# Optimization experiments

Measured on AMD Instinct MI355X. Metric: run time of the kernel, lower is better.

## Reference

```python
import jax, jax.numpy as jnp
import numpy as np

N = 50000   # nodes
E = 800000  # edges (avg degree 16)
G = 64      # graphs in batch


def setup_inputs() -> dict:
    key = jax.random.key(0)
    ks = jax.random.split(key, 32)
    w = lambda k, shape, s=0.05: (jax.random.normal(k, shape, jnp.float32) * s)
    inp = {}
    inp["x"] = jax.random.normal(ks[0], (N, 3), jnp.float32)
    inp["edge_index"] = jax.random.randint(ks[1], (2, E), 0, N)
    inp["batch"] = jnp.sort(jax.random.randint(ks[2], (N,), 0, G))
    # TransformerConv 1: in=3, heads=2, d=32 -> out 64 (concat)
    inp["Wq1"] = w(ks[3], (3, 64));  inp["bq1"] = w(ks[4], (64,))
    inp["Wk1"] = w(ks[5], (3, 64));  inp["bk1"] = w(ks[6], (64,))
    inp["Wv1"] = w(ks[7], (3, 64));  inp["bv1"] = w(ks[8], (64,))
    inp["Ws1"] = w(ks[9], (3, 64));  inp["bs1"] = w(ks[10], (64,))
    # TransformerConv 2: in=64, heads=2, d=64 -> out 128 (concat)
    inp["Wq2"] = w(ks[11], (64, 128)); inp["bq2"] = w(ks[12], (128,))
    inp["Wk2"] = w(ks[13], (64, 128)); inp["bk2"] = w(ks[14], (128,))
    inp["Wv2"] = w(ks[15], (64, 128)); inp["bv2"] = w(ks[16], (128,))
    inp["Ws2"] = w(ks[17], (64, 128)); inp["bs2"] = w(ks[18], (128,))
    # MLP head
    inp["W1"] = w(ks[19], (128, 32)); inp["b1"] = w(ks[20], (32,))
    inp["W2"] = w(ks[21], (32, 128)); inp["b2"] = w(ks[22], (128,))
    inp["W3"] = w(ks[23], (128, 40)); inp["b3"] = w(ks[24], (40,))
    return inp


def _transformer_conv(x, src, dst, Wq, bq, Wk, bk, Wv, bv, Ws, bs, H, d):
    """PyG TransformerConv (concat=True, root_weight=True, beta=False)."""
    n = x.shape[0]
    q = (x @ Wq + bq).reshape(n, H, d)
    k = (x @ Wk + bk).reshape(n, H, d)
    v = (x @ Wv + bv).reshape(n, H, d)
    # per-edge attention logits: q_i . k_j / sqrt(d), i=dst, j=src  -> [E, H]
    s = (q[dst] * k[src]).sum(-1) / jnp.sqrt(jnp.float32(d))
    # segment softmax over edges grouped by destination node
    m = jax.ops.segment_max(s, dst, num_segments=n)
    m = jnp.where(jnp.isfinite(m), m, 0.0)
    e = jnp.exp(s - m[dst])
    denom = jax.ops.segment_sum(e, dst, num_segments=n)
    alpha = e / jnp.maximum(denom[dst], 1e-16)
    # scatter-add weighted values
    out = jax.ops.segment_sum(alpha[:, :, None] * v[src], dst, num_segments=n)
    return out.reshape(n, H * d) + x @ Ws + bs  # skip connection


def reference(x, edge_index, batch,
              Wq1, bq1, Wk1, bk1, Wv1, bv1, Ws1, bs1,
              Wq2, bq2, Wk2, bk2, Wv2, bv2, Ws2, bs2,
              W1, b1, W2, b2, W3, b3):
    src, dst = edge_index[0], edge_index[1]
    h = jax.nn.relu(_transformer_conv(x, src, dst, Wq1, bq1, Wk1, bk1,
                                      Wv1, bv1, Ws1, bs1, 2, 32))
    h = jax.nn.relu(_transformer_conv(h, src, dst, Wq2, bq2, Wk2, bk2,
                                      Wv2, bv2, Ws2, bs2, 2, 64))
    # global max pool over graphs
    p = jax.ops.segment_max(h, batch, num_segments=G)
    p = jnp.where(jnp.isfinite(p), p, 0.0)
    x_latent = jax.nn.relu(p @ W1 + b1)
    y = jax.nn.relu(x_latent @ W2 + b2)
    return (y @ W3 + b3, x_latent)
```

## Files before the change

### kernel.cpp

```cpp
#include <hip/hip_runtime.h>
#include <hip/hip_bf16.h>

typedef short s16x8 __attribute__((ext_vector_type(8)));
typedef float f32x4 __attribute__((ext_vector_type(4)));

#define LOG2E 1.4426950408889634f

__device__ __forceinline__ float bfl(unsigned w) { return __uint_as_float(w << 16); }
__device__ __forceinline__ float bfh(unsigned w) { return __uint_as_float(w & 0xffff0000u); }
__device__ __forceinline__ unsigned f2bf(float f) {
    unsigned u = __float_as_uint(f);
    return (u + 0x7fffu + ((u >> 16) & 1u)) >> 16;
}

__global__ void deg_kernel(const int* __restrict__ dst, int* __restrict__ deg, int E) {
    int e = blockIdx.x * blockDim.x + threadIdx.x;
    if (e < E) atomicAdd(&deg[dst[e]], 1);
}

__global__ void scan_reduce(const int* __restrict__ deg, int* __restrict__ bsum, int n) {
    __shared__ int sh[256];
    int t = threadIdx.x;
    int i = blockIdx.x * 256 + t;
    sh[t] = (i < n) ? deg[i] : 0;
    __syncthreads();
    for (int s = 128; s > 0; s >>= 1) {
        if (t < s) sh[t] += sh[t + s];
        __syncthreads();
    }
    if (t == 0) bsum[blockIdx.x] = sh[0];
}

__global__ void scan_blocks(const int* __restrict__ bsum, int* __restrict__ boff,
                            int nb, int* __restrict__ off, int n) {
    __shared__ int sh[256];
    int t = threadIdx.x;
    int v = (t < nb) ? bsum[t] : 0;
    sh[t] = v;
    __syncthreads();
    for (int d = 1; d < 256; d <<= 1) {
        int x = (t >= d) ? sh[t - d] : 0;
        __syncthreads();
        sh[t] += x;
        __syncthreads();
    }
    if (t < nb) boff[t] = sh[t] - v;
    if (t == 255) off[n] = sh[255];
}

__global__ void scan_apply(const int* __restrict__ deg, const int* __restrict__ boff,
                           int* __restrict__ off, int* __restrict__ cursor, int n) {
    __shared__ int sh[256];
    int t = threadIdx.x;
    int i = blockIdx.x * 256 + t;
    int v = (i < n) ? deg[i] : 0;
    sh[t] = v;
    __syncthreads();
    for (int d = 1; d < 256; d <<= 1) {
        int x = (t >= d) ? sh[t - d] : 0;
        __syncthreads();
        sh[t] += x;
        __syncthreads();
    }
    int ex = sh[t] - v + boff[blockIdx.x];
    if (i < n) {
        off[i] = ex;
        cursor[i] = ex;
    }
}

__global__ void scatter_kernel(const int* __restrict__ src, const int* __restrict__ dst,
                               int* __restrict__ cursor, int* __restrict__ srcs, int E) {
    int e = blockIdx.x * blockDim.x + threadIdx.x;
    if (e < E) {
        int p = atomicAdd(&cursor[dst[e]], 1);
        srcs[p] = src[e];
    }
}

__global__ void prep1(const float* __restrict__ Wq, const float* __restrict__ bq,
                      const float* __restrict__ Wk, float* __restrict__ c1) {
    int t = threadIdx.x;
    if (t < 18) {
        int h = t / 9, rr = t % 9, r = rr / 3, rp = rr % 3;
        float s = 0.f;
        for (int d = 0; d < 32; ++d) s += Wq[r * 64 + h * 32 + d] * Wk[rp * 64 + h * 32 + d];
        c1[t] = s;
    } else if (t < 24) {
        int u = t - 18, h = u / 3, rp = u % 3;
        float s = 0.f;
        for (int d = 0; d < 32; ++d) s += bq[h * 32 + d] * Wk[rp * 64 + h * 32 + d];
        c1[t] = s;
    }
}

__global__ __launch_bounds__(256) void attn1f(
        const float* __restrict__ x, const float* __restrict__ c1,
        const float* __restrict__ Wv, const float* __restrict__ bv,
        const float* __restrict__ Ws, const float* __restrict__ bs,
        const int* __restrict__ off, const int* __restrict__ srcs,
        unsigned* __restrict__ h1b, int n) {
    int lane = threadIdx.x & 63;
    int g = lane >> 2, sl = lane & 3;
    int i = (blockIdx.x * (blockDim.x >> 6) + (threadIdx.x >> 6)) * 16 + g;
    bool act = i < n;
    int ic = act ? i : 0;
    float x0 = x[ic * 3], x1 = x[ic * 3 + 1], x2 = x[ic * 3 + 2];
    float y0[3], y1[3];
#pragma unroll
    for (int rp = 0; rp < 3; ++rp) {
        y0[rp] = x0 * c1[rp] + x1 * c1[3 + rp] + x2 * c1[6 + rp] + c1[18 + rp];
        y1[rp] = x0 * c1[9 + rp] + x1 * c1[12 + rp] + x2 * c1[15 + rp] + c1[21 + rp];
    }
    const float SC = 0.17677669529663688f * LOG2E;
    int e0 = act ? off[ic] : 0, e1 = act ? off[ic + 1] : 0;
    float d0 = 0.f, d1 = 0.f;
    float a0x = 0.f, a0y = 0.f, a0z = 0.f, a1x = 0.f, a1y = 0.f, a1z = 0.f;
    for (int e = e0 + sl; e < e1; e += 4) {
        int j = srcs[e];
        float xj0 = x[j * 3], xj1 = x[j * 3 + 1], xj2 = x[j * 3 + 2];
        float p0 = exp2f((y0[0] * xj0 + y0[1] * xj1 + y0[2] * xj2) * SC);
        float p1 = exp2f((y1[0] * xj0 + y1[1] * xj1 + y1[2] * xj2) * SC);
        d0 += p0; a0x += p0 * xj0; a0y += p0 * xj1; a0z += p0 * xj2;
        d1 += p1; a1x += p1 * xj0; a1y += p1 * xj1; a1z += p1 * xj2;
    }
#pragma unroll
    for (int mask = 1; mask <= 2; mask <<= 1) {
        d0 += __shfl_xor(d0, mask); d1 += __shfl_xor(d1, mask);
        a0x += __shfl_xor(a0x, mask); a0y += __shfl_xor(a0y, mask);
        a0z += __shfl_xor(a0z, mask); a1x += __shfl_xor(a1x, mask);
        a1y += __shfl_xor(a1y, mask); a1z += __shfl_xor(a1z, mask);
    }
    if (!act) return;
    int head = sl >> 1;
    float dh = head ? d1 : d0;
    float inv = 1.f / fmaxf(dh, 1e-16f);
    float sg = dh > 0.f ? 1.f : 0.f;
    float Ax = (head ? a1x : a0x) * inv;
    float Ay = (head ? a1y : a0y) * inv;
    float Az = (head ? a1z : a0z) * inv;
    unsigned pk[8];
#pragma unroll
    for (int u = 0; u < 8; ++u) {
        int c = sl * 16 + 2 * u;
        float2 wv0 = *(const float2*)&Wv[c], wv1 = *(const float2*)&Wv[64 + c],
               wv2 = *(const float2*)&Wv[128 + c];
        float2 ws0 = *(const float2*)&Ws[c], ws1 = *(const float2*)&Ws[64 + c],
               ws2 = *(const float2*)&Ws[128 + c];
        float2 bbv = *(const float2*)&bv[c];
        float2 bbs = *(const float2*)&bs[c];
        float v0 = Ax * wv0.x + Ay * wv1.x + Az * wv2.x + sg * bbv.x +
                   x0 * ws0.x + x1 * ws1.x + x2 * ws2.x + bbs.x;
        float v1 = Ax * wv0.y + Ay * wv1.y + Az * wv2.y + sg * bbv.y +
                   x0 * ws0.y + x1 * ws1.y + x2 * ws2.y + bbs.y;
        pk[u] = f2bf(fmaxf(v0, 0.f)) | (f2bf(fmaxf(v1, 0.f)) << 16);
    }
    uint4 pa = {pk[0], pk[1], pk[2], pk[3]};
    uint4 pb = {pk[4], pk[5], pk[6], pk[7]};
    *(uint4*)&h1b[(size_t)i * 32 + sl * 8] = pa;
    *(uint4*)&h1b[(size_t)i * 32 + sl * 8 + 4] = pb;
}

__global__ void prep2(const float* __restrict__ Wq, const float* __restrict__ bq,
                      const float* __restrict__ Wk, float* __restrict__ Mcat,
                      float* __restrict__ wcat) {
    int t = blockIdx.x * blockDim.x + threadIdx.x;
    if (t < 8192) {
        int k = t >> 7, cc = t & 127, h = cc >> 6, kp = cc & 63;
        float s = 0.f;
        for (int d = 0; d < 64; ++d) s += Wq[k * 128 + h * 64 + d] * Wk[kp * 128 + h * 64 + d];
        Mcat[k * 128 + cc] = s;
    } else if (t < 8320) {
        int cc = t - 8192, h = cc >> 6, kp = cc & 63;
        float s = 0.f;
        for (int d = 0; d < 64; ++d) s += bq[h * 64 + d] * Wk[kp * 128 + h * 64 + d];
        wcat[cc] = s;
    }
}

__global__ void prep2p(const float* __restrict__ Mcat, ushort* __restrict__ bfragY) {
    int t = blockIdx.x * blockDim.x + threadIdx.x;
    int frag = t >> 6, l = t & 63;
    int ct = frag >> 1, ks = frag & 1;
    int c = ct * 16 + (l & 15);
    int kbase = ks * 32 + ((l >> 4) << 3);
#pragma unroll
    for (int e = 0; e < 8; ++e)
        bfragY[(size_t)frag * 512 + l * 8 + e] = (ushort)f2bf(Mcat[(kbase + e) * 128 + c]);
}

__global__ __launch_bounds__(256) void lin2Y(const ushort* __restrict__ h1b,
                                             const ushort* __restrict__ bfragY,
                                             const float* __restrict__ wcat,
                                             float* __restrict__ Yp, int n) {
    int node0 = blockIdx.x * 16;
    int w = threadIdx.x >> 6, l = threadIdx.x & 63;
    int arow = node0 + (l & 15);
    if (arow >= n) arow = n - 1;
    s16x8 a0 = *(const s16x8*)&h1b[(size_t)arow * 64 + ((l >> 4) << 3)];
    s16x8 a1 = *(const s16x8*)&h1b[(size_t)arow * 64 + 32 + ((l >> 4) << 3)];
    int cl = l & 15;
#pragma unroll
    for (int qq = 0; qq < 2; ++qq) {
        int ct = w * 2 + qq;
        s16x8 b0 = *(const s16x8*)&bfragY[(size_t)(ct * 2 + 0) * 512 + l * 8];
        s16x8 b1 = *(const s16x8*)&bfragY[(size_t)(ct * 2 + 1) * 512 + l * 8];
        f32x4 acc = {0.f, 0.f, 0.f, 0.f};
        acc = __builtin_amdgcn_mfma_f32_16x16x32_bf16(a0, b0, acc, 0, 0, 0);
        acc = __builtin_amdgcn_mfma_f32_16x16x32_bf16(a1, b1, acc, 0, 0, 0);
        int cg = ct * 16 + cl;
        float bb = wcat[cg];
#pragma unroll
        for (int r = 0; r < 4; ++r) {
            int node = node0 + ((l >> 4) << 2) + r;
            if (node < n) Yp[(size_t)node * 128 + cg] = acc[r] + bb;
        }
    }
}

__global__ void attn2_kernel(const float* __restrict__ Yp, const unsigned* __restrict__ h1u,
                             const int* __restrict__ off, const int* __restrict__ srcs,
                             unsigned* __restrict__ a01, float2* __restrict__ sig2, int n) {
    int i = blockIdx.x * (blockDim.x >> 6) + (threadIdx.x >> 6);
    int lane = threadIdx.x & 63;
    if (i >= n) return;
    int og = lane >> 3, sl = lane & 7;
    int e0 = off[i], e1 = off[i + 1];
    const float SC = 0.125f * LOG2E;
    float4 ya0 = *(const float4*)&Yp[(size_t)i * 128 + 8 * sl];
    float4 ya1 = *(const float4*)&Yp[(size_t)i * 128 + 8 * sl + 4];
    float4 yb0 = *(const float4*)&Yp[(size_t)i * 128 + 64 + 8 * sl];
    float4 yb1 = *(const float4*)&Yp[(size_t)i * 128 + 64 + 8 * sl + 4];
    float d0 = 0.f, d1 = 0.f;
    float a0[8] = {0.f, 0.f, 0.f, 0.f, 0.f, 0.f, 0.f, 0.f};
    float a1[8] = {0.f, 0.f, 0.f, 0.f, 0.f, 0.f, 0.f, 0.f};
    for (int e = e0 + og; e < e1; e += 8) {
        int j = srcs[e];
        uint4 hb = *(const uint4*)&h1u[(size_t)j * 32 + 4 * sl];
        float h[8];
        h[0] = bfl(hb.x); h[1] = bfh(hb.x); h[2] = bfl(hb.y); h[3] = bfh(hb.y);
        h[4] = bfl(hb.z); h[5] = bfh(hb.z); h[6] = bfl(hb.w); h[7] = bfh(hb.w);
        float t0 = ya0.x * h[0] + ya0.y * h[1] + ya0.z * h[2] + ya0.w * h[3] +
                   ya1.x * h[4] + ya1.y * h[5] + ya1.z * h[6] + ya1.w * h[7];
        float t1 = yb0.x * h[0] + yb0.y * h[1] + yb0.z * h[2] + yb0.w * h[3] +
                   yb1.x * h[4] + yb1.y * h[5] + yb1.z * h[6] + yb1.w * h[7];
        t0 += __shfl_xor(t0, 1); t0 += __shfl_xor(t0, 2); t0 += __shfl_xor(t0, 4);
        t1 += __shfl_xor(t1, 1); t1 += __shfl_xor(t1, 2); t1 += __shfl_xor(t1, 4);
        float p0 = exp2f(t0 * SC);
        float p1 = exp2f(t1 * SC);
        d0 += p0;
        d1 += p1;
#pragma unroll
        for (int k = 0; k < 8; ++k) {
            a0[k] += p0 * h[k];
            a1[k] += p1 * h[k];
        }
    }
#pragma unroll
    for (int mask = 8; mask <= 32; mask <<= 1) {
        d0 += __shfl_xor(d0, mask);
        d1 += __shfl_xor(d1, mask);
#pragma unroll
        for (int k = 0; k < 8; ++k) {
            a0[k] += __shfl_xor(a0[k], mask);
            a1[k] += __shfl_xor(a1[k], mask);
        }
    }
    if (og == 0) {
        float i0 = 1.f / fmaxf(d0, 1e-16f), i1 = 1.f / fmaxf(d1, 1e-16f);
        uint4 pa, pb;
        pa.x = f2bf(a0[0] * i0) | (f2bf(a0[1] * i0) << 16);
        pa.y = f2bf(a0[2] * i0) | (f2bf(a0[3] * i0) << 16);
        pa.z = f2bf(a0[4] * i0) | (f2bf(a0[5] * i0) << 16);
        pa.w = f2bf(a0[6] * i0) | (f2bf(a0[7] * i0) << 16);
        pb.x = f2bf(a1[0] * i1) | (f2bf(a1[1] * i1) << 16);
        pb.y = f2bf(a1[2] * i1) | (f2bf(a1[3] * i1) << 16);
        pb.z = f2bf(a1[4] * i1) | (f2bf(a1[5] * i1) << 16);
        pb.w = f2bf(a1[6] * i1) | (f2bf(a1[7] * i1) << 16);
        *(uint4*)&a01[(size_t)i * 64 + 4 * sl] = pa;
        *(uint4*)&a01[(size_t)i * 64 + 32 + 4 * sl] = pb;
        if (sl == 0) {
            float2 sg = {d0 > 0.f ? 1.f : 0.f, d1 > 0.f ? 1.f : 0.f};
            sig2[i] = sg;
        }
    }
}

__global__ void prep_epi(const float* __restrict__ Wv, const float* __restrict__ Ws,
                         ushort* __restrict__ B192) {
    int t = blockIdx.x * blockDim.x + threadIdx.x;
    int frag = t >> 6, l = t & 63;
    int ct = frag / 6, ks = frag % 6;
    int c = ct * 16 + (l & 15);
    int kbase = ks * 32 + ((l >> 4) << 3);
#pragma unroll
    for (int e = 0; e < 8; ++e) {
        int k = kbase + e;
        float v;
        if (k < 64) v = (c < 64) ? Wv[k * 128 + c] : 0.f;
        else if (k < 128) v = (c >= 64) ? Wv[(k - 64) * 128 + c] : 0.f;
        else v = Ws[(k - 128) * 128 + c];
        B192[(size_t)frag * 512 + l * 8 + e] = (ushort)f2bf(v);
    }
}

__global__ __launch_bounds__(256) void epi2(
        const ushort* __restrict__ a01, const ushort* __restrict__ h1b,
        const ushort* __restrict__ B192, const float* __restrict__ bv,
        const float* __restrict__ bs, const float* __restrict__ sig2,
        const int* __restrict__ batch, unsigned* __restrict__ pool, int n) {
    __shared__ float po[16][128];
    __shared__ int pg[16];
    int node0 = blockIdx.x * 16;
    int w = threadIdx.x >> 6, l = threadIdx.x & 63;
    int arow = node0 + (l & 15);
    int arc = (arow < n) ? arow : (n - 1);
    int koff = (l >> 4) << 3;
    s16x8 af[6];
    af[0] = *(const s16x8*)&a01[(size_t)arc * 128 + 0 + koff];
    af[1] = *(const s16x8*)&a01[(size_t)arc * 128 + 32 + koff];
    af[2] = *(const s16x8*)&a01[(size_t)arc * 128 + 64 + koff];
    af[3] = *(const s16x8*)&a01[(size_t)arc * 128 + 96 + koff];
    af[4] = *(const s16x8*)&h1b[(size_t)arc * 64 + 0 + koff];
    af[5] = *(const s16x8*)&h1b[(size_t)arc * 64 + 32 + koff];
    if (threadIdx.x < 16)
        pg[threadIdx.x] = (node0 + threadIdx.x < n) ? batch[node0 + threadIdx.x] : -1;
    int cl = l & 15;
#pragma unroll
    for (int qq = 0; qq < 2; ++qq) {
        int ct = w * 2 + qq;
        f32x4 acc = {0.f, 0.f, 0.f, 0.f};
#pragma unroll
        for (int ks = 0; ks < 6; ++ks) {
            s16x8 b = *(const s16x8*)&B192[(size_t)(ct * 6 + ks) * 512 + l * 8];
            acc = __builtin_amdgcn_mfma_f32_16x16x32_bf16(af[ks], b, acc, 0, 0, 0);
        }
        int cg = ct * 16 + cl;
        int head = cg >> 6;
        float bbs = bs[cg], bbv = bv[cg];
#pragma unroll
        for (int r = 0; r < 4; ++r) {
            int row = ((l >> 4) << 2) + r;
            int node = node0 + row;
            float sg = (node < n) ? sig2[node * 2 + head] : 0.f;
            po[row][cg] = fmaxf(acc[r] + sg * bbv + bbs, 0.f);
        }
    }
    __syncthreads();
    int t = threadIdx.x;
    if (t < 128) {
        int curg = -1;
        float mx = 0.f;
        for (int r = 0; r < 16; ++r) {
            int g = pg[r];
            if (g < 0) continue;
            if (g != curg) {
                if (curg >= 0) atomicMax(&pool[(size_t)curg * 128 + t], __float_as_uint(mx));
                curg = g;
                mx = 0.f;
            }
            mx = fmaxf(mx, po[r][t]);
        }
        if (curg >= 0) atomicMax(&pool[(size_t)curg * 128 + t], __float_as_uint(mx));
    }
}

__global__ void head_kernel(const unsigned* __restrict__ pbits,
                            const float* __restrict__ W1, const float* __restrict__ b1,
                            const float* __restrict__ W2, const float* __restrict__ b2,
                            const float* __restrict__ W3, const float* __restrict__ b3,
                            float* __restrict__ out, int G) {
    int g = blockIdx.x;
    int t = threadIdx.x;
    __shared__ float ps[128], xl[32], y[128];
    ps[t] = __uint_as_float(pbits[g * 128 + t]);
    __syncthreads();
    if (t < 32) {
        float a = b1[t];
        for (int k = 0; k < 128; ++k) a += ps[k] * W1[k * 32 + t];
        a = fmaxf(a, 0.f);
        xl[t] = a;
        out[G * 40 + g * 32 + t] = a;
    }
    __syncthreads();
    {
        float a = b2[t];
        for (int k = 0; k < 32; ++k) a += xl[k] * W2[k * 128 + t];
        y[t] = fmaxf(a, 0.f);
    }
    __syncthreads();
    if (t < 40) {
        float a = b3[t];
        for (int k = 0; k < 128; ++k) a += y[k] * W3[k * 40 + t];
        out[g * 40 + t] = a;
    }
}

extern "C" void kernel_launch(void* const* d_in, const int* in_sizes, int n_in,
                              void* d_out, int out_size, void* d_ws, size_t ws_size,
                              hipStream_t stream) {
    const float* x = (const float*)d_in[0];
    const int* eidx = (const int*)d_in[1];
    const int* batch = (const int*)d_in[2];
    const float *Wq1 = (const float*)d_in[3], *bq1 = (const float*)d_in[4];
    const float *Wk1 = (const float*)d_in[5], *bk1 = (const float*)d_in[6];
    const float *Wv1 = (const float*)d_in[7], *bv1 = (const float*)d_in[8];
    const float *Ws1 = (const float*)d_in[9], *bs1 = (const float*)d_in[10];
    const float *Wq2 = (const float*)d_in[11], *bq2 = (const float*)d_in[12];
    const float *Wk2 = (const float*)d_in[13], *bk2 = (const float*)d_in[14];
    const float *Wv2 = (const float*)d_in[15], *bv2 = (const float*)d_in[16];
    const float *Ws2 = (const float*)d_in[17], *bs2 = (const float*)d_in[18];
    const float *W1 = (const float*)d_in[19], *b1 = (const float*)d_in[20];
    const float *W2 = (const float*)d_in[21], *b2 = (const float*)d_in[22];
    const float *W3 = (const float*)d_in[23], *b3 = (const float*)d_in[24];
    (void)bk1; (void)bk2;

    const int N = in_sizes[0] / 3;
    const int E = in_sizes[1] / 2;
    const int G = out_size / 72;
    const int* esrc = eidx;
    const int* edst = eidx + E;
    const int NB = (N + 255) / 256;

    char* w = (char*)d_ws;
    size_t o = 0;
    auto alloc = [&](size_t bytes) {
        void* p = w + o;
        o = (o + bytes + 255) & ~(size_t)255;
        return p;
    };
    float* c1buf = (float*)alloc(24 * 4);
    float* Mcat = (float*)alloc(64 * 128 * 4);
    float* wcat = (float*)alloc(128 * 4);
    ushort* bfragY = (ushort*)alloc(16 * 512 * 2);
    ushort* B192 = (ushort*)alloc(48 * 512 * 2);
    unsigned* h1b = (unsigned*)alloc((size_t)N * 32 * 4);
    float* Yp = (float*)alloc((size_t)N * 128 * 4);
    unsigned* a01 = (unsigned*)alloc((size_t)N * 64 * 4);
    float* sig2 = (float*)alloc((size_t)N * 2 * 4);
    int* deg = (int*)alloc((size_t)N * 4);
    int* off = (int*)alloc((size_t)(N + 1) * 4);
    int* cursor = (int*)alloc((size_t)N * 4);
    int* srcs = (int*)alloc((size_t)E * 4);
    unsigned* pool = (unsigned*)alloc((size_t)G * 128 * 4);
    int* bsum = (int*)alloc(256 * 4);
    int* boff = (int*)alloc(256 * 4);
    (void)ws_size;

    hipMemsetAsync(deg, 0, (size_t)N * 4, stream);
    deg_kernel<<<(E + 255) / 256, 256, 0, stream>>>(edst, deg, E);
    scan_reduce<<<NB, 256, 0, stream>>>(deg, bsum, N);
    scan_blocks<<<1, 256, 0, stream>>>(bsum, boff, NB, off, N);
    scan_apply<<<NB, 256, 0, stream>>>(deg, boff, off, cursor, N);
    scatter_kernel<<<(E + 255) / 256, 256, 0, stream>>>(esrc, edst, cursor, srcs, E);

    prep1<<<1, 64, 0, stream>>>(Wq1, bq1, Wk1, c1buf);
    prep2<<<33, 256, 0, stream>>>(Wq2, bq2, Wk2, Mcat, wcat);
    prep2p<<<4, 256, 0, stream>>>(Mcat, bfragY);
    prep_epi<<<12, 256, 0, stream>>>(Wv2, Ws2, B192);

    attn1f<<<(N + 63) / 64, 256, 0, stream>>>(x, c1buf, Wv1, bv1, Ws1, bs1, off, srcs,
                                              h1b, N);

    lin2Y<<<(N + 15) / 16, 256, 0, stream>>>((const ushort*)h1b, bfragY, wcat, Yp, N);
    attn2_kernel<<<(N + 3) / 4, 256, 0, stream>>>(Yp, h1b, off, srcs, a01,
                                                  (float2*)sig2, N);
    hipMemsetAsync(pool, 0, (size_t)G * 128 * 4, stream);
    epi2<<<(N + 15) / 16, 256, 0, stream>>>((const ushort*)a01, (const ushort*)h1b, B192,
                                            bv2, bs2, sig2, batch, pool, N);

    head_kernel<<<G, 128, 0, stream>>>(pool, W1, b1, W2, b2, W3, b3, (float*)d_out, G);
}
```

Baseline: 209.9 us.

## Merge weight-prep kernels and memsets into one launch; widen attn1 lanes per node

Folds prep1, prep2, prep2p, prep_epi and both memsets (deg and pool) into a single prep_all kernel, so several small launches and the intermediate Mcat buffer go away. The bf16 MFMA fragments are now written directly from the computed dot products. Separately, attn1f now uses 8 lanes per node instead of 4, which halves nodes per wave and launches twice as many blocks. This gives more parallelism over each node's edges at the cost of an extra shuffle stage. Pool zeroing now happens before the CSR build rather than just before epi2, which still precedes its use.

```diff
diff --git a/kernel.cpp b/kernel.cpp
--- a/kernel.cpp
+++ b/kernel.cpp
@@ -78,19 +78,66 @@
     }
 }
 
-__global__ void prep1(const float* __restrict__ Wq, const float* __restrict__ bq,
-                      const float* __restrict__ Wk, float* __restrict__ c1) {
-    int t = threadIdx.x;
-    if (t < 18) {
-        int h = t / 9, rr = t % 9, r = rr / 3, rp = rr % 3;
+__global__ void prep_all(const float* __restrict__ Wq1, const float* __restrict__ bq1,
+                         const float* __restrict__ Wk1,
+                         const float* __restrict__ Wq2, const float* __restrict__ bq2,
+                         const float* __restrict__ Wk2,
+                         const float* __restrict__ Wv2, const float* __restrict__ Ws2,
+                         float* __restrict__ c1, float* __restrict__ wcat,
+                         ushort* __restrict__ bfragY, ushort* __restrict__ B192,
+                         int* __restrict__ deg, unsigned* __restrict__ pool,
+                         int n, int nbdeg, int poolsz) {
+    int b = blockIdx.x, t = threadIdx.x;
+    if (b == 0) {
+        if (t < 18) {
+            int h = t / 9, rr = t % 9, r = rr / 3, rp = rr % 3;
+            float s = 0.f;
+            for (int d = 0; d < 32; ++d)
+                s += Wq1[r * 64 + h * 32 + d] * Wk1[rp * 64 + h * 32 + d];
+            c1[t] = s;
+        } else if (t < 24) {
+            int u = t - 18, h = u / 3, rp = u % 3;
+            float s = 0.f;
+            for (int d = 0; d < 32; ++d)
+                s += bq1[h * 32 + d] * Wk1[rp * 64 + h * 32 + d];
+            c1[t] = s;
+        } else if (t >= 64 && t < 192) {
+            int cc = t - 64, h = cc >> 6, kp = cc & 63;
+            float s = 0.f;
+            for (int d = 0; d < 64; ++d)
+                s += bq2[h * 64 + d] * Wk2[kp * 128 + h * 64 + d];
+            wcat[cc] = s;
+        }
+    } else if (b < 33) {
+        int idx = (b - 1) * 256 + t;
+        int k = idx >> 7, cc = idx & 127, h = cc >> 6, kp = cc & 63;
         float s = 0.f;
-        for (int d = 0; d < 32; ++d) s += Wq[r * 64 + h * 32 + d] * Wk[rp * 64 + h * 32 + d];
-        c1[t] = s;
-    } else if (t < 24) {
-        int u = t - 18, h = u / 3, rp = u % 3;
-        float s = 0.f;
-        for (int d = 0; d < 32; ++d) s += bq[h * 32 + d] * Wk[rp * 64 + h * 32 + d];
-        c1[t] = s;
+        for (int d = 0; d < 64; ++d)
+            s += Wq2[k * 128 + h * 64 + d] * Wk2[kp * 128 + h * 64 + d];
+        int frag = ((cc >> 4) << 1) | (k >> 5);
+        int l = (cc & 15) | (((k >> 3) & 3) << 4);
+        bfragY[(size_t)frag * 512 + l * 8 + (k & 7)] = (ushort)f2bf(s);
+    } else if (b < 45) {
+        int tt = (b - 33) * 256 + t;
+        int frag = tt >> 6, l = tt & 63;
+        int ct = frag / 6, ks = frag % 6;
+        int c = ct * 16 + (l & 15);
+        int kbase = ks * 32 + ((l >> 4) << 3);
+#pragma unroll
+        for (int e = 0; e < 8; ++e) {
+            int k = kbase + e;
+            float v;
+            if (k < 64) v = (c < 64) ? Wv2[k * 128 + c] : 0.f;
+            else if (k < 128) v = (c >= 64) ? Wv2[(k - 64) * 128 + c] : 0.f;
+            else v = Ws2[(k - 128) * 128 + c];
+            B192[(size_t)frag * 512 + l * 8 + e] = (ushort)f2bf(v);
+        }
+    } else if (b < 45 + nbdeg) {
+        int i = (b - 45) * 256 + t;
+        if (i < n) deg[i] = 0;
+    } else {
+        int i = (b - 45 - nbdeg) * 256 + t;
+        if (i < poolsz) pool[i] = 0;
     }
 }
 
@@ -101,8 +148,8 @@
         const int* __restrict__ off, const int* __restrict__ srcs,
         unsigned* __restrict__ h1b, int n) {
     int lane = threadIdx.x & 63;
-    int g = lane >> 2, sl = lane & 3;
-    int i = (blockIdx.x * (blockDim.x >> 6) + (threadIdx.x >> 6)) * 16 + g;
+    int g = lane >> 3, sl = lane & 7;
+    int i = (blockIdx.x * (blockDim.x >> 6) + (threadIdx.x >> 6)) * 8 + g;
     bool act = i < n;
     int ic = act ? i : 0;
     float x0 = x[ic * 3], x1 = x[ic * 3 + 1], x2 = x[ic * 3 + 2];
@@ -116,7 +163,7 @@
     int e0 = act ? off[ic] : 0, e1 = act ? off[ic + 1] : 0;
     float d0 = 0.f, d1 = 0.f;
     float a0x = 0.f, a0y = 0.f, a0z = 0.f, a1x = 0.f, a1y = 0.f, a1z = 0.f;
-    for (int e = e0 + sl; e < e1; e += 4) {
+    for (int e = e0 + sl; e < e1; e += 8) {
         int j = srcs[e];
         float xj0 = x[j * 3], xj1 = x[j * 3 + 1], xj2 = x[j * 3 + 2];
         float p0 = exp2f((y0[0] * xj0 + y0[1] * xj1 + y0[2] * xj2) * SC);
@@ -125,24 +172,24 @@
         d1 += p1; a1x += p1 * xj0; a1y += p1 * xj1; a1z += p1 * xj2;
     }
 #pragma unroll
-    for (int mask = 1; mask <= 2; mask <<= 1) {
+    for (int mask = 1; mask <= 4; mask <<= 1) {
         d0 += __shfl_xor(d0, mask); d1 += __shfl_xor(d1, mask);
         a0x += __shfl_xor(a0x, mask); a0y += __shfl_xor(a0y, mask);
         a0z += __shfl_xor(a0z, mask); a1x += __shfl_xor(a1x, mask);
         a1y += __shfl_xor(a1y, mask); a1z += __shfl_xor(a1z, mask);
     }
     if (!act) return;
-    int head = sl >> 1;
+    int head = sl >> 2;
     float dh = head ? d1 : d0;
     float inv = 1.f / fmaxf(dh, 1e-16f);
     float sg = dh > 0.f ? 1.f : 0.f;
     float Ax = (head ? a1x : a0x) * inv;
     float Ay = (head ? a1y : a0y) * inv;
     float Az = (head ? a1z : a0z) * inv;
-    unsigned pk[8];
-#pragma unroll
-    for (int u = 0; u < 8; ++u) {
-        int c = sl * 16 + 2 * u;
+    unsigned pk[4];
+#pragma unroll
+    for (int u = 0; u < 4; ++u) {
+        int c = sl * 8 + 2 * u;
         float2 wv0 = *(const float2*)&Wv[c], wv1 = *(const float2*)&Wv[64 + c],
                wv2 = *(const float2*)&Wv[128 + c];
         float2 ws0 = *(const float2*)&Ws[c], ws1 = *(const float2*)&Ws[64 + c],
@@ -156,37 +203,7 @@
         pk[u] = f2bf(fmaxf(v0, 0.f)) | (f2bf(fmaxf(v1, 0.f)) << 16);
     }
     uint4 pa = {pk[0], pk[1], pk[2], pk[3]};
-    uint4 pb = {pk[4], pk[5], pk[6], pk[7]};
-    *(uint4*)&h1b[(size_t)i * 32 + sl * 8] = pa;
-    *(uint4*)&h1b[(size_t)i * 32 + sl * 8 + 4] = pb;
-}
-
-__global__ void prep2(const float* __restrict__ Wq, const float* __restrict__ bq,
-                      const float* __restrict__ Wk, float* __restrict__ Mcat,
-                      float* __restrict__ wcat) {
-    int t = blockIdx.x * blockDim.x + threadIdx.x;
-    if (t < 8192) {
-        int k = t >> 7, cc = t & 127, h = cc >> 6, kp = cc & 63;
-        float s = 0.f;
-        for (int d = 0; d < 64; ++d) s += Wq[k * 128 + h * 64 + d] * Wk[kp * 128 + h * 64 + d];
-        Mcat[k * 128 + cc] = s;
-    } else if (t < 8320) {
-        int cc = t - 8192, h = cc >> 6, kp = cc & 63;
-        float s = 0.f;
-        for (int d = 0; d < 64; ++d) s += bq[h * 64 + d] * Wk[kp * 128 + h * 64 + d];
-        wcat[cc] = s;
-    }
-}
-
-__global__ void prep2p(const float* __restrict__ Mcat, ushort* __restrict__ bfragY) {
-    int t = blockIdx.x * blockDim.x + threadIdx.x;
-    int frag = t >> 6, l = t & 63;
-    int ct = frag >> 1, ks = frag & 1;
-    int c = ct * 16 + (l & 15);
-    int kbase = ks * 32 + ((l >> 4) << 3);
-#pragma unroll
-    for (int e = 0; e < 8; ++e)
-        bfragY[(size_t)frag * 512 + l * 8 + e] = (ushort)f2bf(Mcat[(kbase + e) * 128 + c]);
+    *(uint4*)&h1b[(size_t)i * 32 + sl * 4] = pa;
 }
 
 __global__ __launch_bounds__(256) void lin2Y(const ushort* __restrict__ h1b,
@@ -286,24 +303,6 @@
     }
 }
 
-__global__ void prep_epi(const float* __restrict__ Wv, const float* __restrict__ Ws,
-                         ushort* __restrict__ B192) {
-    int t = blockIdx.x * blockDim.x + threadIdx.x;
-    int frag = t >> 6, l = t & 63;
-    int ct = frag / 6, ks = frag % 6;
-    int c = ct * 16 + (l & 15);
-    int kbase = ks * 32 + ((l >> 4) << 3);
-#pragma unroll
-    for (int e = 0; e < 8; ++e) {
-        int k = kbase + e;
-        float v;
-        if (k < 64) v = (c < 64) ? Wv[k * 128 + c] : 0.f;
-        else if (k < 128) v = (c >= 64) ? Wv[(k - 64) * 128 + c] : 0.f;
-        else v = Ws[(k - 128) * 128 + c];
-        B192[(size_t)frag * 512 + l * 8 + e] = (ushort)f2bf(v);
-    }
-}
-
 __global__ __launch_bounds__(256) void epi2(
         const ushort* __restrict__ a01, const ushort* __restrict__ h1b,
         const ushort* __restrict__ B192, const float* __restrict__ bv,
@@ -421,6 +420,8 @@
     const int* esrc = eidx;
     const int* edst = eidx + E;
     const int NB = (N + 255) / 256;
+    const int POOLSZ = G * 128;
+    const int PB = (POOLSZ + 255) / 256;
 
     char* w = (char*)d_ws;
     size_t o = 0;
@@ -430,7 +431,6 @@
         return p;
     };
     float* c1buf = (float*)alloc(24 * 4);
-    float* Mcat = (float*)alloc(64 * 128 * 4);
     float* wcat = (float*)alloc(128 * 4);
     ushort* bfragY = (ushort*)alloc(16 * 512 * 2);
     ushort* B192 = (ushort*)alloc(48 * 512 * 2);
@@ -442,30 +442,27 @@
     int* off = (int*)alloc((size_t)(N + 1) * 4);
     int* cursor = (int*)alloc((size_t)N * 4);
     int* srcs = (int*)alloc((size_t)E * 4);
-    unsigned* pool = (unsigned*)alloc((size_t)G * 128 * 4);
+    unsigned* pool = (unsigned*)alloc((size_t)POOLSZ * 4);
     int* bsum = (int*)alloc(256 * 4);
     int* boff = (int*)alloc(256 * 4);
     (void)ws_size;
 
-    hipMemsetAsync(deg, 0, (size_t)N * 4, stream);
+    prep_all<<<45 + NB + PB, 256, 0, stream>>>(Wq1, bq1, Wk1, Wq2, bq2, Wk2, Wv2, Ws2,
+                                               c1buf, wcat, bfragY, B192, deg, pool,
+                                               N, NB, POOLSZ);
+
     deg_kernel<<<(E + 255) / 256, 256, 0, stream>>>(edst, deg, E);
     scan_reduce<<<NB, 256, 0, stream>>>(deg, bsum, N);
     scan_blocks<<<1, 256, 0, stream>>>(bsum, boff, NB, off, N);
     scan_apply<<<NB, 256, 0, stream>>>(deg, boff, off, cursor, N);
     scatter_kernel<<<(E + 255) / 256, 256, 0, stream>>>(esrc, edst, cursor, srcs, E);
 
-    prep1<<<1, 64, 0, stream>>>(Wq1, bq1, Wk1, c1buf);
-    prep2<<<33, 256, 0, stream>>>(Wq2, bq2, Wk2, Mcat, wcat);
-    prep2p<<<4, 256, 0, stream>>>(Mcat, bfragY);
-    prep_epi<<<12, 256, 0, stream>>>(Wv2, Ws2, B192);
-
-    attn1f<<<(N + 63) / 64, 256, 0, stream>>>(x, c1buf, Wv1, bv1, Ws1, bs1, off, srcs,
+    attn1f<<<(N + 31) / 32, 256, 0, stream>>>(x, c1buf, Wv1, bv1, Ws1, bs1, off, srcs,
                                               h1b, N);
 
     lin2Y<<<(N + 15) / 16, 256, 0, stream>>>((const ushort*)h1b, bfragY, wcat, Yp, N);
     attn2_kernel<<<(N + 3) / 4, 256, 0, stream>>>(Yp, h1b, off, srcs, a01,
                                                   (float2*)sig2, N);
-    hipMemsetAsync(pool, 0, (size_t)G * 128 * 4, stream);
     epi2<<<(N + 15) / 16, 256, 0, stream>>>((const ushort*)a01, (const ushort*)h1b, B192,
                                             bv2, bs2, sig2, batch, pool, N);
 
```

New measurement: 193.8 us. -7.7%, faster.
